# Performance work log

Hardware: AMD Instinct MI355X
Metric: run time of the kernel (lower is better)

## Reference

```python
import jax, jax.numpy as jnp
import numpy as np

B, T, C_EMB, HEAD = 8, 2048, 1024, 64

def setup_inputs() -> dict:
    key = jax.random.key(0)
    kx, kq, kk, kv = jax.random.split(key, 4)
    x = jax.random.normal(kx, (B, T, C_EMB), dtype=jnp.float32)
    s = 1.0 / np.sqrt(C_EMB)
    Wq = jax.random.normal(kq, (C_EMB, HEAD), dtype=jnp.float32) * s
    Wk = jax.random.normal(kk, (C_EMB, HEAD), dtype=jnp.float32) * s
    Wv = jax.random.normal(kv, (C_EMB, HEAD), dtype=jnp.float32) * s
    return {"x": x, "Wq": Wq, "Wk": Wk, "Wv": Wv}


def _apply_rotary(q, k):
    # q, k: [B, T, D] with D = head_size; matches torch apply_rotary_emb
    D = q.shape[-1]
    pos = jnp.arange(q.shape[1], dtype=jnp.float32)                # [T]
    dim_arr = jnp.arange(0, D, 2, dtype=jnp.float32)               # [D/2]
    freqs = 10000.0 ** (-dim_arr / D)                              # [D/2]
    theta = pos[:, None] * freqs[None, :]                          # [T, D/2]
    cos = jnp.concatenate([jnp.cos(theta), jnp.cos(theta)], -1)[None]  # [1,T,D]
    sin = jnp.concatenate([jnp.sin(theta), jnp.sin(theta)], -1)[None]

    def rot(v):
        v1, v2 = v[..., : D // 2], v[..., D // 2 :]
        return jnp.concatenate([-v2, v1], axis=-1)

    return q * cos + rot(q) * sin, k * cos + rot(k) * sin


def reference(x, Wq, Wk, Wv):
    Bx, Tx, Cx = x.shape
    q = x @ Wq  # [B,T,H]
    k = x @ Wk
    v = x @ Wv
    q, k = _apply_rotary(q, k)
    # NOTE: original scales by C**-0.5 where C = n_embd, not head_size
    scale = Cx ** (-0.5)
    wei = jnp.einsum("bqd,bkd->bqk", q, k) * scale                 # [B,T,T]
    causal = jnp.tril(jnp.ones((Tx, Tx), dtype=bool))
    wei = jnp.where(causal[None], wei, -jnp.inf)
    wei = jax.nn.softmax(wei, axis=-1)
    out = jnp.einsum("bqk,bkd->bqd", wei, v)                       # [B,T,H]
    return out
```

## Files before the change

### kernel.cpp

```cpp
#include <hip/hip_runtime.h>

typedef __bf16 bf16x8 __attribute__((ext_vector_type(8)));
typedef float f32x4 __attribute__((ext_vector_type(4)));
typedef unsigned short u16;

#define MFMA __builtin_amdgcn_mfma_f32_16x16x32_bf16

__device__ __forceinline__ u16 f2bf_bits(float f) {
  unsigned u = __builtin_bit_cast(unsigned, f);
  u = (u + 0x7fffu + ((u >> 16) & 1u)) >> 16;
  return (u16)u;
}
__device__ __forceinline__ __bf16 f2bf(float f) {
  u16 b = f2bf_bits(f);
  return __builtin_bit_cast(__bf16, b);
}
__device__ __forceinline__ float bf2f(u16 b) {
  return __builtin_bit_cast(float, (unsigned)b << 16);
}

__device__ __forceinline__ void barrier_lds_only() {
  asm volatile("s_waitcnt lgkmcnt(0)" ::: "memory");
  __builtin_amdgcn_s_barrier();
}

__device__ __forceinline__ int swz_off(int row, int col) {
  return row * 64 + ((((col >> 3) ^ row) & 7) << 3) + (col & 7);
}
__device__ __forceinline__ bf16x8 lds_read8(const __bf16* buf, int row, int col) {
  return *(const bf16x8*)(buf + (row * 64 + ((((col >> 3) ^ row) & 7) << 3)));
}
__device__ __forceinline__ void lds_write8(__bf16* buf, int row, int col, bf16x8 v) {
  *(bf16x8*)(buf + (row * 64 + ((((col >> 3) ^ row) & 7) << 3))) = v;
}

__global__ __launch_bounds__(256) void prep_w_kernel(
    const float* __restrict__ Wq, const float* __restrict__ Wk,
    const float* __restrict__ Wv, u16* __restrict__ wtg) {
  __shared__ float tile[64][65];
  const int tid = threadIdx.x;
  const int kt = blockIdx.x & 15;
  const int ct = blockIdx.x >> 4;
  const float* W = (ct == 0) ? Wq : ((ct == 1) ? Wk : Wv);
  const int k0 = kt * 64;
#pragma unroll
  for (int i = 0; i < 16; ++i) {
    int row = i * 4 + (tid >> 6), col = tid & 63;
    tile[row][col] = W[(size_t)(k0 + row) * 64 + col];
  }
  __syncthreads();
#pragma unroll
  for (int i = 0; i < 16; ++i) {
    int col = i * 4 + (tid >> 6), krow = tid & 63;
    wtg[(size_t)(ct * 64 + col) * 1024 + k0 + krow] = f2bf_bits(tile[krow][col]);
  }
}

__device__ __forceinline__ void rope2(f32x4& lo, f32x4& hi, int i, float t_base) {
  float f = __expf(-(float)i * 0.28782313662425572f);
  const float inv2pi = 0.15915494309189535f;
#pragma unroll
  for (int r = 0; r < 4; ++r) {
    float rev = (t_base + (float)r) * f * inv2pi;
    rev = __builtin_amdgcn_fractf(rev);
    float sn = __builtin_amdgcn_sinf(rev);
    float cs = __builtin_amdgcn_cosf(rev);
    float L = lo[r], H = hi[r];
    lo[r] = L * cs - H * sn;
    hi[r] = H * cs + L * sn;
  }
}

__global__ __launch_bounds__(512) void qkv_rope_kernel(
    const float* __restrict__ x, const u16* __restrict__ wtg,
    u16* __restrict__ qg, u16* __restrict__ kg, u16* __restrict__ vtg) {
  __shared__ __bf16 xbuf[2][64 * 64];
  __shared__ __bf16 wbuf[2][192 * 64];
  const int tid = threadIdx.x;
  const int w = tid >> 6, l = tid & 63;
  const int wrg = w & 1;
  const int wcg = w >> 1;
  const int lr = l & 15, lg = l >> 4;
  const int r0 = blockIdx.x * 64;
  const int b = r0 >> 11, t0 = r0 & 2047;
  constexpr int TM4[4][3] = {{0, 2, 8}, {1, 3, 9}, {4, 6, 10}, {5, 7, 11}};

  f32x4 acc[2][3];
#pragma unroll
  for (int rg = 0; rg < 2; ++rg)
#pragma unroll
    for (int j = 0; j < 3; ++j) acc[rg][j] = (f32x4){0.f, 0.f, 0.f, 0.f};

  const int srow = tid >> 3, sc8 = tid & 7;
  const float* xbase = x + (size_t)(r0 + srow) * 1024 + sc8 * 8;

  float4 xA0, xA1, xB0, xB1, xC0, xC1;
  bf16x8 swr[3];

  auto loadW = [&](int k0) {
#pragma unroll
    for (int s = 0; s < 3; ++s) {
      int id = tid + s * 512;
      swr[s] = *(const bf16x8*)(wtg + (size_t)(id >> 3) * 1024 + k0 + (id & 7) * 8);
    }
  };
  auto writeW = [&](int bsel) {
#pragma unroll
    for (int s = 0; s < 3; ++s) {
      int id = tid + s * 512;
      lds_write8(wbuf[bsel], id >> 3, (id & 7) * 8, swr[s]);
    }
  };
  auto loadX = [&](int step, int sel) {
    const float* p = xbase + (size_t)step * 64;
    if (sel == 0)      { xA0 = *(const float4*)p; xA1 = *(const float4*)(p + 4); }
    else if (sel == 1) { xB0 = *(const float4*)p; xB1 = *(const float4*)(p + 4); }
    else               { xC0 = *(const float4*)p; xC1 = *(const float4*)(p + 4); }
  };
  auto writeX = [&](int bsel, int sel) {
    float4 a0, a1;
    if (sel == 0)      { a0 = xA0; a1 = xA1; }
    else if (sel == 1) { a0 = xB0; a1 = xB1; }
    else               { a0 = xC0; a1 = xC1; }
    bf16x8 v;
    v[0] = f2bf(a0.x); v[1] = f2bf(a0.y); v[2] = f2bf(a0.z); v[3] = f2bf(a0.w);
    v[4] = f2bf(a1.x); v[5] = f2bf(a1.y); v[6] = f2bf(a1.z); v[7] = f2bf(a1.w);
    lds_write8(xbuf[bsel], srow, sc8 * 8, v);
  };

  loadX(0, 0);
  loadW(0);
  writeX(0, 0);
  writeW(0);
  loadX(1, 1);
  loadX(2, 2);
  barrier_lds_only();

#pragma unroll
  for (int s = 0; s < 16; ++s) {
    const int cur = s & 1;
    if (s < 13) loadX(s + 3, s % 3);
    if (s < 15) loadW((s + 1) * 64);
#pragma unroll
    for (int kk = 0; kk < 2; ++kk) {
      bf16x8 a0 = lds_read8(xbuf[cur], wrg * 32 + lr, kk * 32 + lg * 8);
      bf16x8 a1 = lds_read8(xbuf[cur], wrg * 32 + 16 + lr, kk * 32 + lg * 8);
#pragma unroll
      for (int j = 0; j < 3; ++j) {
        bf16x8 bb = lds_read8(wbuf[cur], TM4[wcg][j] * 16 + lr, kk * 32 + lg * 8);
        acc[0][j] = MFMA(a0, bb, acc[0][j], 0, 0, 0);
        acc[1][j] = MFMA(a1, bb, acc[1][j], 0, 0, 0);
      }
    }
    if (s < 15) {
      writeX(cur ^ 1, (s + 1) % 3);
      writeW(cur ^ 1);
      barrier_lds_only();
    }
  }

  const int ph = (wcg & 1) * 16 + lr;
#pragma unroll
  for (int rg = 0; rg < 2; ++rg) {
    const int rowb = wrg * 32 + rg * 16 + lg * 4;
    const float t_base = (float)(t0 + rowb);
    rope2(acc[rg][0], acc[rg][1], ph, t_base);
    if (wcg < 2) {
#pragma unroll
      for (int r = 0; r < 4; ++r) {
        size_t rowo = (size_t)(r0 + rowb + r) * 64;
        qg[rowo + ph] = f2bf_bits(acc[rg][0][r] * 0.03125f);
        qg[rowo + 32 + ph] = f2bf_bits(acc[rg][1][r] * 0.03125f);
      }
    } else {
#pragma unroll
      for (int r = 0; r < 4; ++r) {
        size_t rowo = (size_t)(r0 + rowb + r) * 64;
        kg[rowo + ph] = f2bf_bits(acc[rg][0][r]);
        kg[rowo + 32 + ph] = f2bf_bits(acc[rg][1][r]);
      }
    }
    {
      const int d = (TM4[wcg][2] - 8) * 16 + lr;
      ushort4 uv;
      uv.x = f2bf_bits(acc[rg][2][0]);
      uv.y = f2bf_bits(acc[rg][2][1]);
      uv.z = f2bf_bits(acc[rg][2][2]);
      uv.w = f2bf_bits(acc[rg][2][3]);
      *(ushort4*)(vtg + (size_t)(b * 64 + d) * 2048 + t0 + rowb) = uv;
    }
  }
}

__global__ __launch_bounds__(256) void attn_part_kernel(
    const u16* __restrict__ qg, const u16* __restrict__ kg,
    const u16* __restrict__ vtg, u16* __restrict__ opart,
    float* __restrict__ lpart, float* __restrict__ out, int CT, int NCH) {
  const int idx = blockIdx.x;
  const int b = idx / (32 * NCH);
  const int rem = idx % (32 * NCH);
  const int qt = rem / NCH, ch = rem % NCH;
  const int t0v = ch * CT;
  if (t0v > qt) return;
  const int t1v = min(qt + 1, t0v + CT);
  const int nv = qt / CT + 1;

  __shared__ __bf16 kbuf[2][64 * 64];
  __shared__ __bf16 vbuf[2][64 * 64];
  __shared__ __bf16 pbuf[4 * 16 * 64];
  const int tid = threadIdx.x;
  const int w = tid >> 6, l = tid & 63;
  const int lr = l & 15, lg = l >> 4;
  const int q0 = qt * 64;
  const float NEG_INF = -__builtin_inff();

  const u16* qrow = qg + (size_t)(b * 2048 + q0 + w * 16 + lr) * 64;
  bf16x8 qf0 = *(const bf16x8*)(qrow + lg * 8);
  bf16x8 qf1 = *(const bf16x8*)(qrow + 32 + lg * 8);

  bf16x8 kr[2], vr[2];
  auto stage_load = [&](int c) {
#pragma unroll
    for (int s = 0; s < 2; ++s) {
      int id = tid + s * 256;
      int row = id >> 3, c8 = id & 7;
      kr[s] = *(const bf16x8*)(kg + (size_t)(b * 2048 + c * 64 + row) * 64 + c8 * 8);
      vr[s] = *(const bf16x8*)(vtg + (size_t)(b * 64 + row) * 2048 + c * 64 + c8 * 8);
    }
  };
  auto stage_write = [&](int bsel) {
#pragma unroll
    for (int s = 0; s < 2; ++s) {
      int id = tid + s * 256;
      int row = id >> 3, c8 = id & 7;
      lds_write8(kbuf[bsel], row, c8 * 8, kr[s]);
      lds_write8(vbuf[bsel], row, c8 * 8, vr[s]);
    }
  };

  f32x4 acc_o[4];
#pragma unroll
  for (int n = 0; n < 4; ++n) acc_o[n] = (f32x4){0.f, 0.f, 0.f, 0.f};
  float l_p[4] = {0.f, 0.f, 0.f, 0.f};

  stage_load(t0v);
  stage_write(0);
  __syncthreads();

  for (int c = t0v; c < t1v; ++c) {
    const int cur = (c - t0v) & 1;
    const bool more = (c + 1 < t1v);
    if (more) stage_load(c + 1);

    f32x4 s4[4];
#pragma unroll
    for (int nt = 0; nt < 4; ++nt) {
      bf16x8 k0 = lds_read8(kbuf[cur], nt * 16 + lr, lg * 8);
      bf16x8 k1 = lds_read8(kbuf[cur], nt * 16 + lr, 32 + lg * 8);
      f32x4 t = (f32x4){0.f, 0.f, 0.f, 0.f};
      t = MFMA(qf0, k0, t, 0, 0, 0);
      t = MFMA(qf1, k1, t, 0, 0, 0);
      s4[nt] = t;
    }
    if (c == qt) {
#pragma unroll
      for (int nt = 0; nt < 4; ++nt)
#pragma unroll
        for (int r = 0; r < 4; ++r) {
          int kv = nt * 16 + lr, qq = w * 16 + lg * 4 + r;
          if (kv > qq) s4[nt][r] = NEG_INF;
        }
    }
    __bf16* pw = pbuf + w * (16 * 64);
#pragma unroll
    for (int nt = 0; nt < 4; ++nt)
#pragma unroll
      for (int r = 0; r < 4; ++r) {
        float p = __expf(s4[nt][r] - 8.0f);
        l_p[r] += p;
        pw[swz_off(lg * 4 + r, nt * 16 + lr)] = f2bf(p);
      }
#pragma unroll
    for (int h = 0; h < 2; ++h) {
      bf16x8 pf = lds_read8(pw, lr, h * 32 + lg * 8);
#pragma unroll
      for (int nt = 0; nt < 4; ++nt) {
        bf16x8 vf = lds_read8(vbuf[cur], nt * 16 + lr, h * 32 + lg * 8);
        acc_o[nt] = MFMA(pf, vf, acc_o[nt], 0, 0, 0);
      }
    }
    if (more) {
      stage_write(cur ^ 1);
      __syncthreads();
    }
  }

  float lsum[4];
#pragma unroll
  for (int r = 0; r < 4; ++r) {
    float s = l_p[r];
    s += __shfl_xor(s, 1);
    s += __shfl_xor(s, 2);
    s += __shfl_xor(s, 4);
    s += __shfl_xor(s, 8);
    lsum[r] = s;
  }

  if (nv == 1) {
#pragma unroll
    for (int r = 0; r < 4; ++r) {
      float inv = 1.0f / lsum[r];
      size_t rowo = (size_t)(b * 2048 + q0 + w * 16 + lg * 4 + r) * 64;
#pragma unroll
      for (int nt = 0; nt < 4; ++nt)
        out[rowo + nt * 16 + lr] = acc_o[nt][r] * inv;
    }
    return;
  }

  const size_t slot = (size_t)(b * 32 + qt) * NCH + ch;
  u16* oslot = opart + slot * 4096;
#pragma unroll
  for (int r = 0; r < 4; ++r) {
    int row = w * 16 + lg * 4 + r;
#pragma unroll
    for (int nt = 0; nt < 4; ++nt)
      oslot[row * 64 + nt * 16 + lr] = f2bf_bits(acc_o[nt][r]);
    if (lr == 0) lpart[slot * 64 + row] = lsum[r];
  }
}

__global__ __launch_bounds__(256) void attn_combine_kernel(
    const u16* __restrict__ opart, const float* __restrict__ lpart,
    float* __restrict__ out, int CT, int NCH) {
  const int bq = blockIdx.x >> 2;
  const int quarter = blockIdx.x & 3;
  const int b = bq >> 5, qt = bq & 31;
  const int nv = qt / CT + 1;
  if (nv == 1) return;
  const int row = quarter * 16 + (threadIdx.x >> 4);
  const int col = (threadIdx.x & 15) * 4;
  const size_t slot0 = (size_t)(b * 32 + qt) * NCH;

  float denom = 0.f;
  float acc[4] = {0.f, 0.f, 0.f, 0.f};
  for (int c = 0; c < nv; ++c) {
    denom += lpart[(slot0 + c) * 64 + row];
    ushort4 pv = *(const ushort4*)(opart + (slot0 + c) * 4096 + row * 64 + col);
    acc[0] += bf2f(pv.x);
    acc[1] += bf2f(pv.y);
    acc[2] += bf2f(pv.z);
    acc[3] += bf2f(pv.w);
  }
  float inv = 1.0f / denom;
  float4 o;
  o.x = acc[0] * inv; o.y = acc[1] * inv; o.z = acc[2] * inv; o.w = acc[3] * inv;
  *(float4*)(out + ((size_t)(b * 2048 + qt * 64 + row)) * 64 + col) = o;
}

extern "C" void kernel_launch(void* const* d_in, const int* in_sizes, int n_in,
                              void* d_out, int out_size, void* d_ws, size_t ws_size,
                              hipStream_t stream) {
  const float* x = (const float*)d_in[0];
  const float* Wq = (const float*)d_in[1];
  const float* Wk = (const float*)d_in[2];
  const float* Wv = (const float*)d_in[3];
  float* out = (float*)d_out;
  char* ws = (char*)d_ws;
  u16* wtg = (u16*)ws;
  u16* qg = (u16*)(ws + 393216);
  u16* kg = (u16*)(ws + 393216 + 2097152);
  u16* vtg = (u16*)(ws + 393216 + 2u * 2097152);
  const size_t base = 393216 + 3u * 2097152;
  int NCH = 8;
  while (NCH > 1 && base + (size_t)256 * NCH * 8448 > ws_size) NCH >>= 1;
  const int CT = 32 / NCH;
  u16* opart = (u16*)(ws + base);
  float* lpart = (float*)(ws + base + (size_t)256 * NCH * 8192);

  prep_w_kernel<<<dim3(48), dim3(256), 0, stream>>>(Wq, Wk, Wv, wtg);
  qkv_rope_kernel<<<dim3(256), dim3(512), 0, stream>>>(x, wtg, qg, kg, vtg);
  attn_part_kernel<<<dim3(8 * 32 * NCH), dim3(256), 0, stream>>>(
      qg, kg, vtg, opart, lpart, out, CT, NCH);
  attn_combine_kernel<<<dim3(256 * 4), dim3(256), 0, stream>>>(opart, lpart, out, CT, NCH);
}
```

Before: 52.64 us.

## Read K and V tiles directly from global memory instead of LDS staging

```diff
diff --git a/kernel.cpp b/kernel.cpp
--- a/kernel.cpp
+++ b/kernel.cpp
@@ -205,8 +205,6 @@
   const int t1v = min(qt + 1, t0v + CT);
   const int nv = qt / CT + 1;
 
-  __shared__ __bf16 kbuf[2][64 * 64];
-  __shared__ __bf16 vbuf[2][64 * 64];
   __shared__ __bf16 pbuf[4 * 16 * 64];
   const int tid = threadIdx.x;
   const int w = tid >> 6, l = tid & 63;
@@ -218,45 +216,23 @@
   bf16x8 qf0 = *(const bf16x8*)(qrow + lg * 8);
   bf16x8 qf1 = *(const bf16x8*)(qrow + 32 + lg * 8);
 
-  bf16x8 kr[2], vr[2];
-  auto stage_load = [&](int c) {
-#pragma unroll
-    for (int s = 0; s < 2; ++s) {
-      int id = tid + s * 256;
-      int row = id >> 3, c8 = id & 7;
-      kr[s] = *(const bf16x8*)(kg + (size_t)(b * 2048 + c * 64 + row) * 64 + c8 * 8);
-      vr[s] = *(const bf16x8*)(vtg + (size_t)(b * 64 + row) * 2048 + c * 64 + c8 * 8);
-    }
-  };
-  auto stage_write = [&](int bsel) {
-#pragma unroll
-    for (int s = 0; s < 2; ++s) {
-      int id = tid + s * 256;
-      int row = id >> 3, c8 = id & 7;
-      lds_write8(kbuf[bsel], row, c8 * 8, kr[s]);
-      lds_write8(vbuf[bsel], row, c8 * 8, vr[s]);
-    }
-  };
+  const u16* kgb = kg + (size_t)(b * 2048) * 64;
+  const u16* vtb = vtg + (size_t)(b * 64) * 2048;
 
   f32x4 acc_o[4];
 #pragma unroll
   for (int n = 0; n < 4; ++n) acc_o[n] = (f32x4){0.f, 0.f, 0.f, 0.f};
   float l_p[4] = {0.f, 0.f, 0.f, 0.f};
 
-  stage_load(t0v);
-  stage_write(0);
-  __syncthreads();
-
   for (int c = t0v; c < t1v; ++c) {
-    const int cur = (c - t0v) & 1;
-    const bool more = (c + 1 < t1v);
-    if (more) stage_load(c + 1);
+    const u16* ktile = kgb + (size_t)c * 64 * 64;
 
     f32x4 s4[4];
 #pragma unroll
     for (int nt = 0; nt < 4; ++nt) {
-      bf16x8 k0 = lds_read8(kbuf[cur], nt * 16 + lr, lg * 8);
-      bf16x8 k1 = lds_read8(kbuf[cur], nt * 16 + lr, 32 + lg * 8);
+      const u16* krow = ktile + (size_t)(nt * 16 + lr) * 64;
+      bf16x8 k0 = *(const bf16x8*)(krow + lg * 8);
+      bf16x8 k1 = *(const bf16x8*)(krow + 32 + lg * 8);
       f32x4 t = (f32x4){0.f, 0.f, 0.f, 0.f};
       t = MFMA(qf0, k0, t, 0, 0, 0);
       t = MFMA(qf1, k1, t, 0, 0, 0);
@@ -285,13 +261,10 @@
       bf16x8 pf = lds_read8(pw, lr, h * 32 + lg * 8);
 #pragma unroll
       for (int nt = 0; nt < 4; ++nt) {
-        bf16x8 vf = lds_read8(vbuf[cur], nt * 16 + lr, h * 32 + lg * 8);
+        bf16x8 vf = *(const bf16x8*)(vtb + (size_t)(nt * 16 + lr) * 2048 +
+                                     c * 64 + h * 32 + lg * 8);
         acc_o[nt] = MFMA(pf, vf, acc_o[nt], 0, 0, 0);
       }
-    }
-    if (more) {
-      stage_write(cur ^ 1);
-      __syncthreads();
     }
   }
 
```

After: 96.29 us. +82.9%, slower.
